# Optimization experiments

Hardware: AMD Instinct MI355X
Metric: run time of the kernel (lower is better)

## Reference

```python
import jax, jax.numpy as jnp
import numpy as np

TAU = 2.0          # LIF membrane time constant
VTH = 1.0          # spike threshold
ALPHA = 2.0        # ATan surrogate default alpha
EPS = 1e-5         # LayerNorm eps


@jax.custom_vjp
def atan_spike(x):
    # Heaviside forward, ATan surrogate gradient backward (spikingjelly surrogate.ATan)
    return (x >= 0.0).astype(x.dtype)

def _spike_fwd(x):
    return atan_spike(x), x

def _spike_bwd(x, g):
    sg = (ALPHA / 2.0) / (1.0 + (jnp.pi / 2.0 * ALPHA * x) ** 2)
    return (g * sg,)

atan_spike.defvjp(_spike_fwd, _spike_bwd)


def lif_scan(xs):
    # xs: [T, B, C]; multi-step LIF with decay_input=True, v_reset=0.0 (hard reset),
    # detach_reset=True (reset path is stop_gradient'ed).
    def step(v, x):
        h = v + (x - v) / TAU                      # charge
        s = atan_spike(h - VTH)                    # fire
        v_new = h * (1.0 - jax.lax.stop_gradient(s))  # hard reset to 0, detached
        return v_new, s
    _, spikes = jax.lax.scan(step, jnp.zeros_like(xs[0]), xs)
    return spikes


def setup_inputs() -> dict:
    key = jax.random.key(0)
    ks = jax.random.split(key, 5)
    B, T, D, H = 32, 2048, 128, 256
    x = jax.random.normal(ks[0], (B, T, D), dtype=jnp.float32)
    W1 = jax.random.normal(ks[1], (H, D), dtype=jnp.float32) * (1.0 / np.sqrt(D))
    b1 = jax.random.normal(ks[2], (H,), dtype=jnp.float32) * 0.02
    W2 = jax.random.normal(ks[3], (D, H), dtype=jnp.float32) * (1.0 / np.sqrt(H))
    b2 = jax.random.normal(ks[4], (D,), dtype=jnp.float32) * 0.02
    ln_w = jnp.ones((D,), dtype=jnp.float32)
    ln_b = jnp.zeros((D,), dtype=jnp.float32)
    return {"x": x, "W1": W1, "b1": b1, "W2": W2, "b2": b2, "ln_w": ln_w, "ln_b": ln_b}


def reference(x, W1, b1, W2, b2, ln_w, ln_b):
    # x: [B, T, D] -> time-major [T, B, D]
    h = jnp.swapaxes(x, 0, 1)
    h = h @ W1.T + b1            # [T, B, H]
    h = lif_scan(h)              # spikes in {0,1}
    h = h @ W2.T + b2            # [T, B, D]
    h = lif_scan(h)
    h = jnp.swapaxes(h, 0, 1)    # back to [B, T, D]
    y = x + h                    # residual
    mu = jnp.mean(y, axis=-1, keepdims=True)
    var = jnp.mean((y - mu) ** 2, axis=-1, keepdims=True)
    return (y - mu) * jax.lax.rsqrt(var + EPS) * ln_w + ln_b
```

## Files before the change

kernel.cpp:

```cpp
#include <hip/hip_runtime.h>


typedef _Float16 half8 __attribute__((ext_vector_type(8)));
typedef float f32x4 __attribute__((ext_vector_type(4)));

#define MFMA_F16(a, b, c) __builtin_amdgcn_mfma_f32_16x16x32_f16(a, b, c, 0, 0, 0)

__device__ __forceinline__ unsigned short h2u(_Float16 h) {
    union { _Float16 h; unsigned short u; } x; x.h = h; return x.u;
}

__global__ __launch_bounds__(256) void wsplit_kernel(
    const float* __restrict__ W1, const float* __restrict__ W2,
    unsigned short* __restrict__ out)
{
    int i = blockIdx.x * 256 + threadIdx.x;
    const float* src = (i < 32768) ? W1 : W2;
    unsigned short* dst = out + ((i < 32768) ? 0 : 2 * 32768);
    int j = i & 32767;
    float v = src[j];
    _Float16 a = (_Float16)v;
    float r = v - (float)a;
    _Float16 b = (_Float16)r;
    dst[j] = h2u(a); dst[32768 + j] = h2u(b);
}

__global__ __launch_bounds__(512, 1) void mega_kernel(
    const float* __restrict__ X,
    const unsigned short* __restrict__ W1a, const unsigned short* __restrict__ W1b,
    const unsigned short* __restrict__ W2a, const unsigned short* __restrict__ W2b,
    const float* __restrict__ b1, const float* __restrict__ b2,
    const float* __restrict__ lnw, const float* __restrict__ lnb,
    float* __restrict__ out)
{
    __shared__ __align__(16) float buf1[32 * 258];
    __shared__ __align__(16) unsigned short buf2[2 * 32 * 136];
    _Float16* xA0 = (_Float16*)buf2;
    _Float16* xA1 = (_Float16*)(buf2 + 32 * 136);
    _Float16* spH = (_Float16*)buf2;
    unsigned short* spU = buf2;

    const int tid = threadIdx.x;
    const int lane = tid & 63;
    const int w = tid >> 6;
    const int fr = lane & 15;
    const int fo8 = (lane >> 4) * 8;
    const int qr = (lane >> 4) * 4;
    const int b = blockIdx.y;
    const int t0 = blockIdx.x * 256;
    const int s0 = (blockIdx.x == 0) ? 4 : 0;

    half8 b1f[2][4][2];
#pragma unroll
    for (int j = 0; j < 2; ++j) {
        const size_t n = (size_t)(32 * w + 16 * j + fr) * 128;
#pragma unroll
        for (int k0 = 0; k0 < 4; ++k0) {
            b1f[j][k0][0] = *(const half8*)&W1a[n + k0 * 32 + fo8];
            b1f[j][k0][1] = *(const half8*)&W1b[n + k0 * 32 + fo8];
        }
    }
    half8 b2f[8][2];
    {
        const size_t d = (size_t)(16 * w + fr) * 256;
#pragma unroll
        for (int ks = 0; ks < 8; ++ks) {
            b2f[ks][0] = *(const half8*)&W2a[d + ks * 32 + fo8];
            b2f[ks][1] = *(const half8*)&W2b[d + ks * 32 + fo8];
        }
    }
    const float b1v0 = b1[32 * w + fr];
    const float b1v1 = b1[32 * w + 16 + fr];
    const float b2v  = b2[16 * w + fr];
    const float2 wv = *(const float2*)(lnw + lane * 2);
    const float2 bbv = *(const float2*)(lnb + lane * 2);

    float v1 = 0.0f, v2 = 0.0f;

    for (int s = s0; s < 12; ++s) {
        const int tbase = t0 - 128 + s * 32;
        const bool mainsub = (s >= 4);

#pragma unroll
        for (int qq = 0; qq < 2; ++qq) {
            int idx4 = qq * 512 + tid;
            int row = idx4 >> 5;
            int c4 = (idx4 & 31) * 4;
            float4 xv = *(const float4*)&X[(size_t)(b * 2048 + tbase + row) * 128 + c4];
            _Float16 a0 = (_Float16)xv.x; _Float16 e0 = (_Float16)(xv.x - (float)a0);
            _Float16 a1 = (_Float16)xv.y; _Float16 e1 = (_Float16)(xv.y - (float)a1);
            _Float16 a2 = (_Float16)xv.z; _Float16 e2 = (_Float16)(xv.z - (float)a2);
            _Float16 a3 = (_Float16)xv.w; _Float16 e3 = (_Float16)(xv.w - (float)a3);
            ushort4 ua = {h2u(a0), h2u(a1), h2u(a2), h2u(a3)};
            ushort4 ub = {h2u(e0), h2u(e1), h2u(e2), h2u(e3)};
            *(ushort4*)&buf2[row * 136 + c4] = ua;
            *(ushort4*)&buf2[32 * 136 + row * 136 + c4] = ub;
        }
        __syncthreads();

        {
            f32x4 acc1[2][2];
#pragma unroll
            for (int i = 0; i < 2; ++i)
#pragma unroll
                for (int j = 0; j < 2; ++j) acc1[i][j] = (f32x4){0.f, 0.f, 0.f, 0.f};
#pragma unroll
            for (int k0 = 0; k0 < 4; ++k0) {
                half8 a1r[2], a2r[2];
#pragma unroll
                for (int i = 0; i < 2; ++i) {
                    int off = (i * 16 + fr) * 136 + k0 * 32 + fo8;
                    a1r[i] = *(const half8*)&xA0[off];
                    a2r[i] = *(const half8*)&xA1[off];
                }
#pragma unroll
                for (int i = 0; i < 2; ++i)
#pragma unroll
                    for (int j = 0; j < 2; ++j) {
                        acc1[i][j] = MFMA_F16(a1r[i], b1f[j][k0][0], acc1[i][j]);
                        acc1[i][j] = MFMA_F16(a1r[i], b1f[j][k0][1], acc1[i][j]);
                        acc1[i][j] = MFMA_F16(a2r[i], b1f[j][k0][0], acc1[i][j]);
                    }
            }
#pragma unroll
            for (int i = 0; i < 2; ++i)
#pragma unroll
                for (int j = 0; j < 2; ++j) {
                    int col = 32 * w + 16 * j + fr;
                    float bias = j ? b1v1 : b1v0;
#pragma unroll
                    for (int r = 0; r < 4; ++r)
                        buf1[(i * 16 + qr + r) * 258 + col] = acc1[i][j][r] + bias;
                }
        }
        __syncthreads();

        if (tid < 256) {
            float hh[32];
#pragma unroll
            for (int t = 0; t < 32; ++t) hh[t] = buf1[t * 258 + tid];
#pragma unroll
            for (int t = 0; t < 32; ++t) {
                float h = v1 + (hh[t] - v1) * 0.5f;
                bool sp = (h >= 1.0f);
                v1 = sp ? 0.0f : h;
                spU[t * 264 + tid] = sp ? (unsigned short)0x3C00 : (unsigned short)0;
            }
        }
        __syncthreads();

        {
            f32x4 acc2[2];
            acc2[0] = (f32x4){0.f, 0.f, 0.f, 0.f};
            acc2[1] = (f32x4){0.f, 0.f, 0.f, 0.f};
#pragma unroll
            for (int ks = 0; ks < 8; ++ks) {
                half8 s0r = *(const half8*)&spH[fr * 264 + ks * 32 + fo8];
                half8 s1r = *(const half8*)&spH[(16 + fr) * 264 + ks * 32 + fo8];
                acc2[0] = MFMA_F16(s0r, b2f[ks][0], acc2[0]);
                acc2[0] = MFMA_F16(s0r, b2f[ks][1], acc2[0]);
                acc2[1] = MFMA_F16(s1r, b2f[ks][0], acc2[1]);
                acc2[1] = MFMA_F16(s1r, b2f[ks][1], acc2[1]);
            }
            int col = 16 * w + fr;
#pragma unroll
            for (int i = 0; i < 2; ++i)
#pragma unroll
                for (int r = 0; r < 4; ++r)
                    buf1[(i * 16 + qr + r) * 258 + col] = acc2[i][r] + b2v;
        }
        __syncthreads();

        if (tid < 128) {
            float hh[32];
#pragma unroll
            for (int t = 0; t < 32; ++t) hh[t] = buf1[t * 258 + tid];
#pragma unroll
            for (int t = 0; t < 32; ++t) {
                float h = v2 + (hh[t] - v2) * 0.5f;
                bool sp = (h >= 1.0f);
                v2 = sp ? 0.0f : h;
                if (mainsub) buf1[t * 258 + tid] = sp ? 1.0f : 0.0f;
            }
        }

        if (mainsub) {
            __syncthreads();
#pragma unroll
            for (int rr = 0; rr < 4; ++rr) {
                int row = w * 4 + rr;
                float2 xg = *(const float2*)&X[(size_t)(b * 2048 + tbase + row) * 128 + lane * 2];
                float y0 = xg.x + buf1[row * 258 + lane * 2];
                float y1 = xg.y + buf1[row * 258 + lane * 2 + 1];
                float sum = y0 + y1;
                float ss = y0 * y0 + y1 * y1;
#pragma unroll
                for (int off = 32; off > 0; off >>= 1) {
                    sum += __shfl_xor(sum, off, 64);
                    ss  += __shfl_xor(ss, off, 64);
                }
                float mu = sum * (1.0f / 128.0f);
                float var = ss * (1.0f / 128.0f) - mu * mu;
                float inv = rsqrtf(var + 1e-5f);
                float2 o;
                o.x = (y0 - mu) * inv * wv.x + bbv.x;
                o.y = (y1 - mu) * inv * wv.y + bbv.y;
                *(float2*)(out + (size_t)(b * 2048 + tbase + row) * 128 + lane * 2) = o;
            }
        }
    }
}

extern "C" void kernel_launch(void* const* d_in, const int* in_sizes, int n_in,
                              void* d_out, int out_size, void* d_ws, size_t ws_size,
                              hipStream_t stream)
{
    const float* x   = (const float*)d_in[0];
    const float* W1  = (const float*)d_in[1];
    const float* b1  = (const float*)d_in[2];
    const float* W2  = (const float*)d_in[3];
    const float* b2  = (const float*)d_in[4];
    const float* lnw = (const float*)d_in[5];
    const float* lnb = (const float*)d_in[6];
    float* out = (float*)d_out;

    unsigned short* Wp = (unsigned short*)d_ws;

    wsplit_kernel<<<256, 256, 0, stream>>>(W1, W2, Wp);
    dim3 gM(8, 32);
    mega_kernel<<<gM, 512, 0, stream>>>(x, Wp, Wp + 32768, Wp + 65536, Wp + 98304,
                                        b1, b2, lnw, lnb, out);
}
```

Baseline: 153.3 us.

## Warp-specialize mega kernel to overlap GEMM1 with LIF and GEMM2 stages

Splits the 512-thread block into two roles. Four waves run the LIF scans and GEMM2, while the other four run GEMM1 on the next 16-step chunk, using double-buffered shared memory so stage work overlaps across chunks. It also removes the separate weight-split kernel by splitting W1/W2 into fp16 hi/lo in registers at kernel start, and prefetches X rows into registers ahead of use. The chunk size halves to 16 timesteps, which doubles the number of barriers and sequential steps in exchange for overlap.

```diff
diff --git a/kernel.cpp b/kernel.cpp
--- a/kernel.cpp
+++ b/kernel.cpp
@@ -10,188 +10,238 @@
     union { _Float16 h; unsigned short u; } x; x.h = h; return x.u;
 }
 
-__global__ __launch_bounds__(256) void wsplit_kernel(
-    const float* __restrict__ W1, const float* __restrict__ W2,
-    unsigned short* __restrict__ out)
-{
-    int i = blockIdx.x * 256 + threadIdx.x;
-    const float* src = (i < 32768) ? W1 : W2;
-    unsigned short* dst = out + ((i < 32768) ? 0 : 2 * 32768);
-    int j = i & 32767;
-    float v = src[j];
-    _Float16 a = (_Float16)v;
-    float r = v - (float)a;
-    _Float16 b = (_Float16)r;
-    dst[j] = h2u(a); dst[32768 + j] = h2u(b);
+__device__ __forceinline__ void split8(float4 f0, float4 f1, half8& a, half8& b) {
+    float fs[8] = {f0.x, f0.y, f0.z, f0.w, f1.x, f1.y, f1.z, f1.w};
+    half8 ha, hb;
+#pragma unroll
+    for (int q = 0; q < 8; ++q) {
+        ha[q] = (_Float16)fs[q];
+        hb[q] = (_Float16)(fs[q] - (float)ha[q]);
+    }
+    a = ha; b = hb;
 }
 
 __global__ __launch_bounds__(512, 1) void mega_kernel(
     const float* __restrict__ X,
-    const unsigned short* __restrict__ W1a, const unsigned short* __restrict__ W1b,
-    const unsigned short* __restrict__ W2a, const unsigned short* __restrict__ W2b,
+    const float* __restrict__ W1, const float* __restrict__ W2,
     const float* __restrict__ b1, const float* __restrict__ b2,
     const float* __restrict__ lnw, const float* __restrict__ lnb,
     float* __restrict__ out)
 {
-    __shared__ __align__(16) float buf1[32 * 258];
-    __shared__ __align__(16) unsigned short buf2[2 * 32 * 136];
-    _Float16* xA0 = (_Float16*)buf2;
-    _Float16* xA1 = (_Float16*)(buf2 + 32 * 136);
-    _Float16* spH = (_Float16*)buf2;
-    unsigned short* spU = buf2;
+    __shared__ __align__(16) float hbuf[2][16 * 260];
+    __shared__ __align__(16) unsigned short xabuf[2][2][16 * 136];
 
     const int tid = threadIdx.x;
     const int lane = tid & 63;
     const int w = tid >> 6;
+    const bool isS = (tid < 256);
+    const int sg = w;
+    const int gg = w - 4;
     const int fr = lane & 15;
     const int fo8 = (lane >> 4) * 8;
     const int qr = (lane >> 4) * 4;
     const int b = blockIdx.y;
     const int t0 = blockIdx.x * 256;
-    const int s0 = (blockIdx.x == 0) ? 4 : 0;
-
-    half8 b1f[2][4][2];
-#pragma unroll
-    for (int j = 0; j < 2; ++j) {
-        const size_t n = (size_t)(32 * w + 16 * j + fr) * 128;
-#pragma unroll
-        for (int k0 = 0; k0 < 4; ++k0) {
-            b1f[j][k0][0] = *(const half8*)&W1a[n + k0 * 32 + fo8];
-            b1f[j][k0][1] = *(const half8*)&W1b[n + k0 * 32 + fo8];
-        }
-    }
-    half8 b2f[8][2];
-    {
-        const size_t d = (size_t)(16 * w + fr) * 256;
-#pragma unroll
-        for (int ks = 0; ks < 8; ++ks) {
-            b2f[ks][0] = *(const half8*)&W2a[d + ks * 32 + fo8];
-            b2f[ks][1] = *(const half8*)&W2b[d + ks * 32 + fo8];
-        }
-    }
-    const float b1v0 = b1[32 * w + fr];
-    const float b1v1 = b1[32 * w + 16 + fr];
-    const float b2v  = b2[16 * w + fr];
+    const int s0 = (blockIdx.x == 0) ? 8 : 0;
+
+    const float* __restrict__ xbase = X + (size_t)b * 2048 * 128;
+    float* __restrict__ obase = out + (size_t)b * 2048 * 128;
+
+    half8 wf[32];
+    float bias0[4];
+    if (isS) {
+#pragma unroll
+        for (int j = 0; j < 2; ++j) {
+            const size_t d = (size_t)(32 * sg + 16 * j + fr) * 256;
+#pragma unroll
+            for (int ks = 0; ks < 8; ++ks) {
+                float4 f0 = *(const float4*)&W2[d + ks * 32 + fo8];
+                float4 f1 = *(const float4*)&W2[d + ks * 32 + fo8 + 4];
+                split8(f0, f1, wf[(j * 8 + ks) * 2], wf[(j * 8 + ks) * 2 + 1]);
+            }
+            bias0[j] = b2[32 * sg + 16 * j + fr];
+        }
+    } else {
+#pragma unroll
+        for (int j = 0; j < 4; ++j) {
+            const size_t n = (size_t)(64 * gg + 16 * j + fr) * 128;
+#pragma unroll
+            for (int k0 = 0; k0 < 4; ++k0) {
+                float4 f0 = *(const float4*)&W1[n + k0 * 32 + fo8];
+                float4 f1 = *(const float4*)&W1[n + k0 * 32 + fo8 + 4];
+                split8(f0, f1, wf[(j * 4 + k0) * 2], wf[(j * 4 + k0) * 2 + 1]);
+            }
+            bias0[j] = b1[64 * gg + 16 * j + fr];
+        }
+    }
     const float2 wv = *(const float2*)(lnw + lane * 2);
     const float2 bbv = *(const float2*)(lnb + lane * 2);
 
     float v1 = 0.0f, v2 = 0.0f;
-
-    for (int s = s0; s < 12; ++s) {
-        const int tbase = t0 - 128 + s * 32;
-        const bool mainsub = (s >= 4);
-
-#pragma unroll
-        for (int qq = 0; qq < 2; ++qq) {
-            int idx4 = qq * 512 + tid;
-            int row = idx4 >> 5;
-            int c4 = (idx4 & 31) * 4;
-            float4 xv = *(const float4*)&X[(size_t)(b * 2048 + tbase + row) * 128 + c4];
-            _Float16 a0 = (_Float16)xv.x; _Float16 e0 = (_Float16)(xv.x - (float)a0);
-            _Float16 a1 = (_Float16)xv.y; _Float16 e1 = (_Float16)(xv.y - (float)a1);
-            _Float16 a2 = (_Float16)xv.z; _Float16 e2 = (_Float16)(xv.z - (float)a2);
-            _Float16 a3 = (_Float16)xv.w; _Float16 e3 = (_Float16)(xv.w - (float)a3);
+    float4 pfx[2];
+    const int tg = tid & 255;
+    const int prow = tg >> 5;
+    const int pc4 = (tg & 31) * 4;
+
+    if (!isS) {
+        const int tb0 = t0 - 128 + s0 * 16;
+#pragma unroll
+        for (int q = 0; q < 2; ++q) {
+            float4 xv = *(const float4*)&xbase[(size_t)(tb0 + prow + q * 8) * 128 + pc4];
+            half8 a, e; split8(xv, xv, a, e);
+            _Float16 a0 = (_Float16)xv.x, e0 = (_Float16)(xv.x - (float)a0);
+            _Float16 a1 = (_Float16)xv.y, e1 = (_Float16)(xv.y - (float)a1);
+            _Float16 a2 = (_Float16)xv.z, e2 = (_Float16)(xv.z - (float)a2);
+            _Float16 a3 = (_Float16)xv.w, e3 = (_Float16)(xv.w - (float)a3);
             ushort4 ua = {h2u(a0), h2u(a1), h2u(a2), h2u(a3)};
-            ushort4 ub = {h2u(e0), h2u(e1), h2u(e2), h2u(e3)};
-            *(ushort4*)&buf2[row * 136 + c4] = ua;
-            *(ushort4*)&buf2[32 * 136 + row * 136 + c4] = ub;
-        }
-        __syncthreads();
-
-        {
-            f32x4 acc1[2][2];
-#pragma unroll
-            for (int i = 0; i < 2; ++i)
-#pragma unroll
-                for (int j = 0; j < 2; ++j) acc1[i][j] = (f32x4){0.f, 0.f, 0.f, 0.f};
-#pragma unroll
-            for (int k0 = 0; k0 < 4; ++k0) {
-                half8 a1r[2], a2r[2];
-#pragma unroll
-                for (int i = 0; i < 2; ++i) {
-                    int off = (i * 16 + fr) * 136 + k0 * 32 + fo8;
-                    a1r[i] = *(const half8*)&xA0[off];
-                    a2r[i] = *(const half8*)&xA1[off];
-                }
-#pragma unroll
-                for (int i = 0; i < 2; ++i)
-#pragma unroll
-                    for (int j = 0; j < 2; ++j) {
-                        acc1[i][j] = MFMA_F16(a1r[i], b1f[j][k0][0], acc1[i][j]);
-                        acc1[i][j] = MFMA_F16(a1r[i], b1f[j][k0][1], acc1[i][j]);
-                        acc1[i][j] = MFMA_F16(a2r[i], b1f[j][k0][0], acc1[i][j]);
-                    }
-            }
-#pragma unroll
-            for (int i = 0; i < 2; ++i)
-#pragma unroll
-                for (int j = 0; j < 2; ++j) {
-                    int col = 32 * w + 16 * j + fr;
-                    float bias = j ? b1v1 : b1v0;
-#pragma unroll
-                    for (int r = 0; r < 4; ++r)
-                        buf1[(i * 16 + qr + r) * 258 + col] = acc1[i][j][r] + bias;
-                }
-        }
-        __syncthreads();
-
-        if (tid < 256) {
-            float hh[32];
-#pragma unroll
-            for (int t = 0; t < 32; ++t) hh[t] = buf1[t * 258 + tid];
-#pragma unroll
-            for (int t = 0; t < 32; ++t) {
+            ushort4 ue = {h2u(e0), h2u(e1), h2u(e2), h2u(e3)};
+            *(ushort4*)&xabuf[s0 & 1][0][(prow + q * 8) * 136 + pc4] = ua;
+            *(ushort4*)&xabuf[s0 & 1][1][(prow + q * 8) * 136 + pc4] = ue;
+        }
+#pragma unroll
+        for (int q = 0; q < 2; ++q)
+            pfx[q] = *(const float4*)&xbase[(size_t)(tb0 + 16 + prow + q * 8) * 128 + pc4];
+    }
+    __syncthreads();
+    if (!isS) {
+        const _Float16* xa0 = (const _Float16*)&xabuf[s0 & 1][0][0];
+        const _Float16* xa1 = (const _Float16*)&xabuf[s0 & 1][1][0];
+        f32x4 acc[4];
+#pragma unroll
+        for (int j = 0; j < 4; ++j) acc[j] = (f32x4){0.f, 0.f, 0.f, 0.f};
+#pragma unroll
+        for (int k0 = 0; k0 < 4; ++k0) {
+            half8 a0 = *(const half8*)&xa0[fr * 136 + k0 * 32 + fo8];
+            half8 a1 = *(const half8*)&xa1[fr * 136 + k0 * 32 + fo8];
+#pragma unroll
+            for (int j = 0; j < 4; ++j) {
+                acc[j] = MFMA_F16(a0, wf[(j * 4 + k0) * 2], acc[j]);
+                acc[j] = MFMA_F16(a0, wf[(j * 4 + k0) * 2 + 1], acc[j]);
+                acc[j] = MFMA_F16(a1, wf[(j * 4 + k0) * 2], acc[j]);
+            }
+        }
+#pragma unroll
+        for (int j = 0; j < 4; ++j) {
+            int col = 64 * gg + 16 * j + fr;
+#pragma unroll
+            for (int r = 0; r < 4; ++r)
+                hbuf[s0 & 1][(qr + r) * 260 + col] = acc[j][r] + bias0[j];
+        }
+    }
+    __syncthreads();
+
+    for (int s = s0; s < 24; ++s) {
+        const int tbase = t0 - 128 + s * 16;
+        const bool mainsub = (s >= 8);
+
+        if (isS) {
+            unsigned short* spk = &xabuf[s & 1][0][0];
+            float hh[16];
+#pragma unroll
+            for (int t = 0; t < 16; ++t) hh[t] = hbuf[s & 1][t * 260 + tid];
+#pragma unroll
+            for (int t = 0; t < 16; ++t) {
                 float h = v1 + (hh[t] - v1) * 0.5f;
                 bool sp = (h >= 1.0f);
                 v1 = sp ? 0.0f : h;
-                spU[t * 264 + tid] = sp ? (unsigned short)0x3C00 : (unsigned short)0;
+                spk[t * 264 + tid] = sp ? (unsigned short)0x3C00 : (unsigned short)0;
+            }
+        } else if (s < 23) {
+#pragma unroll
+            for (int q = 0; q < 2; ++q) {
+                float4 xv = pfx[q];
+                _Float16 a0 = (_Float16)xv.x, e0 = (_Float16)(xv.x - (float)a0);
+                _Float16 a1 = (_Float16)xv.y, e1 = (_Float16)(xv.y - (float)a1);
+                _Float16 a2 = (_Float16)xv.z, e2 = (_Float16)(xv.z - (float)a2);
+                _Float16 a3 = (_Float16)xv.w, e3 = (_Float16)(xv.w - (float)a3);
+                ushort4 ua = {h2u(a0), h2u(a1), h2u(a2), h2u(a3)};
+                ushort4 ue = {h2u(e0), h2u(e1), h2u(e2), h2u(e3)};
+                *(ushort4*)&xabuf[(s + 1) & 1][0][(prow + q * 8) * 136 + pc4] = ua;
+                *(ushort4*)&xabuf[(s + 1) & 1][1][(prow + q * 8) * 136 + pc4] = ue;
             }
         }
         __syncthreads();
 
-        {
-            f32x4 acc2[2];
-            acc2[0] = (f32x4){0.f, 0.f, 0.f, 0.f};
-            acc2[1] = (f32x4){0.f, 0.f, 0.f, 0.f};
+        float2 pfln[2];
+        if (mainsub) {
+#pragma unroll
+            for (int rr = 0; rr < 2; ++rr)
+                pfln[rr] = *(const float2*)&xbase[(size_t)(tbase + 2 * w + rr) * 128 + lane * 2];
+        }
+        if (isS) {
+            const _Float16* sp = (const _Float16*)&xabuf[s & 1][0][0];
+            f32x4 acc[2];
+            acc[0] = (f32x4){0.f, 0.f, 0.f, 0.f};
+            acc[1] = (f32x4){0.f, 0.f, 0.f, 0.f};
 #pragma unroll
             for (int ks = 0; ks < 8; ++ks) {
-                half8 s0r = *(const half8*)&spH[fr * 264 + ks * 32 + fo8];
-                half8 s1r = *(const half8*)&spH[(16 + fr) * 264 + ks * 32 + fo8];
-                acc2[0] = MFMA_F16(s0r, b2f[ks][0], acc2[0]);
-                acc2[0] = MFMA_F16(s0r, b2f[ks][1], acc2[0]);
-                acc2[1] = MFMA_F16(s1r, b2f[ks][0], acc2[1]);
-                acc2[1] = MFMA_F16(s1r, b2f[ks][1], acc2[1]);
-            }
-            int col = 16 * w + fr;
-#pragma unroll
-            for (int i = 0; i < 2; ++i)
+                half8 a = *(const half8*)&sp[fr * 264 + ks * 32 + fo8];
+#pragma unroll
+                for (int j = 0; j < 2; ++j) {
+                    acc[j] = MFMA_F16(a, wf[(j * 8 + ks) * 2], acc[j]);
+                    acc[j] = MFMA_F16(a, wf[(j * 8 + ks) * 2 + 1], acc[j]);
+                }
+            }
+#pragma unroll
+            for (int j = 0; j < 2; ++j) {
+                int col = 32 * sg + 16 * j + fr;
 #pragma unroll
                 for (int r = 0; r < 4; ++r)
-                    buf1[(i * 16 + qr + r) * 258 + col] = acc2[i][r] + b2v;
+                    hbuf[s & 1][(qr + r) * 260 + col] = acc[j][r] + bias0[j];
+            }
+        } else if (s < 23) {
+            const _Float16* xa0 = (const _Float16*)&xabuf[(s + 1) & 1][0][0];
+            const _Float16* xa1 = (const _Float16*)&xabuf[(s + 1) & 1][1][0];
+            f32x4 acc[4];
+#pragma unroll
+            for (int j = 0; j < 4; ++j) acc[j] = (f32x4){0.f, 0.f, 0.f, 0.f};
+#pragma unroll
+            for (int k0 = 0; k0 < 4; ++k0) {
+                half8 a0 = *(const half8*)&xa0[fr * 136 + k0 * 32 + fo8];
+                half8 a1 = *(const half8*)&xa1[fr * 136 + k0 * 32 + fo8];
+#pragma unroll
+                for (int j = 0; j < 4; ++j) {
+                    acc[j] = MFMA_F16(a0, wf[(j * 4 + k0) * 2], acc[j]);
+                    acc[j] = MFMA_F16(a0, wf[(j * 4 + k0) * 2 + 1], acc[j]);
+                    acc[j] = MFMA_F16(a1, wf[(j * 4 + k0) * 2], acc[j]);
+                }
+            }
+#pragma unroll
+            for (int j = 0; j < 4; ++j) {
+                int col = 64 * gg + 16 * j + fr;
+#pragma unroll
+                for (int r = 0; r < 4; ++r)
+                    hbuf[(s + 1) & 1][(qr + r) * 260 + col] = acc[j][r] + bias0[j];
+            }
+            if (s < 22) {
+#pragma unroll
+                for (int q = 0; q < 2; ++q)
+                    pfx[q] = *(const float4*)&xbase[(size_t)(tbase + 32 + prow + q * 8) * 128 + pc4];
+            }
         }
         __syncthreads();
 
         if (tid < 128) {
-            float hh[32];
-#pragma unroll
-            for (int t = 0; t < 32; ++t) hh[t] = buf1[t * 258 + tid];
-#pragma unroll
-            for (int t = 0; t < 32; ++t) {
+            float hh[16];
+#pragma unroll
+            for (int t = 0; t < 16; ++t) hh[t] = hbuf[s & 1][t * 260 + tid];
+#pragma unroll
+            for (int t = 0; t < 16; ++t) {
                 float h = v2 + (hh[t] - v2) * 0.5f;
                 bool sp = (h >= 1.0f);
                 v2 = sp ? 0.0f : h;
-                if (mainsub) buf1[t * 258 + tid] = sp ? 1.0f : 0.0f;
+                if (mainsub) hbuf[s & 1][t * 260 + tid] = sp ? 1.0f : 0.0f;
             }
         }
 
         if (mainsub) {
             __syncthreads();
 #pragma unroll
-            for (int rr = 0; rr < 4; ++rr) {
-                int row = w * 4 + rr;
-                float2 xg = *(const float2*)&X[(size_t)(b * 2048 + tbase + row) * 128 + lane * 2];
-                float y0 = xg.x + buf1[row * 258 + lane * 2];
-                float y1 = xg.y + buf1[row * 258 + lane * 2 + 1];
+            for (int rr = 0; rr < 2; ++rr) {
+                int row = 2 * w + rr;
+                float2 s2v = *(const float2*)&hbuf[s & 1][row * 260 + lane * 2];
+                float y0 = pfln[rr].x + s2v.x;
+                float y1 = pfln[rr].y + s2v.y;
                 float sum = y0 + y1;
                 float ss = y0 * y0 + y1 * y1;
 #pragma unroll
@@ -205,7 +255,7 @@
                 float2 o;
                 o.x = (y0 - mu) * inv * wv.x + bbv.x;
                 o.y = (y1 - mu) * inv * wv.y + bbv.y;
-                *(float2*)(out + (size_t)(b * 2048 + tbase + row) * 128 + lane * 2) = o;
+                *(float2*)&obase[(size_t)(tbase + row) * 128 + lane * 2] = o;
             }
         }
     }
@@ -224,10 +274,6 @@
     const float* lnb = (const float*)d_in[6];
     float* out = (float*)d_out;
 
-    unsigned short* Wp = (unsigned short*)d_ws;
-
-    wsplit_kernel<<<256, 256, 0, stream>>>(W1, W2, Wp);
     dim3 gM(8, 32);
-    mega_kernel<<<gM, 512, 0, stream>>>(x, Wp, Wp + 32768, Wp + 65536, Wp + 98304,
-                                        b1, b2, lnw, lnb, out);
-}
+    mega_kernel<<<gM, 512, 0, stream>>>(x, W1, W2, b1, b2, lnw, lnb, out);
+}
```

New measurement: 149.6 us. 1.02x faster.
